# Optimization experiments

Measured on AMD Instinct MI355X. Metric: run time of the kernel, lower is better.

The kernel has to match this reference:

```python
import jax, jax.numpy as jnp
import numpy as np

B, C, CI, H, W = 4, 256, 128, 64, 64  # batch, in_channels, inter_channels, spatial
EPS = 1e-5


def conv1x1(x, w, b):
    # x: [b,c,h,w], w: [o,c], b: [o] -> [b,o,h,w]
    return jnp.einsum('bchw,oc->bohw', x, w) + b[None, :, None, None]


def setup_inputs() -> dict:
    key = jax.random.key(0)
    ks = jax.random.split(key, 16)
    s_in = 1.0 / np.sqrt(C)
    s_mid = 1.0 / np.sqrt(CI)
    inp = {
        'feats_all': jax.random.normal(ks[0], (B, C, H, W), dtype=jnp.float32),
        'human_feats': jax.random.normal(ks[1], (B, C, H, W), dtype=jnp.float32),
        'g_w': jax.random.uniform(ks[2], (CI, C), jnp.float32, -s_in, s_in),
        'g_b': jax.random.uniform(ks[3], (CI,), jnp.float32, -s_in, s_in),
        'theta_w': jax.random.uniform(ks[4], (CI, C), jnp.float32, -s_in, s_in),
        'theta_b': jax.random.uniform(ks[5], (CI,), jnp.float32, -s_in, s_in),
        'phi_w': jax.random.uniform(ks[6], (CI, C), jnp.float32, -s_in, s_in),
        'phi_b': jax.random.uniform(ks[7], (CI,), jnp.float32, -s_in, s_in),
        'human_theta_w': jax.random.uniform(ks[8], (CI, C), jnp.float32, -s_in, s_in),
        'human_theta_b': jax.random.uniform(ks[9], (CI,), jnp.float32, -s_in, s_in),
        'human_phi_w': jax.random.uniform(ks[10], (CI, C), jnp.float32, -s_in, s_in),
        'human_phi_b': jax.random.uniform(ks[11], (CI,), jnp.float32, -s_in, s_in),
        'W_w': jax.random.uniform(ks[12], (C, CI), jnp.float32, -s_mid, s_mid),
        'W_b': jax.random.uniform(ks[13], (C,), jnp.float32, -s_mid, s_mid),
        'bn_gamma': jax.random.normal(ks[14], (C,), dtype=jnp.float32) * 0.1 + 1.0,
        'bn_beta': jax.random.normal(ks[15], (C,), dtype=jnp.float32) * 0.1,
        'bn_mean': jnp.zeros((C,), jnp.float32),
        'bn_var': jnp.ones((C,), jnp.float32),
    }
    return inp


def reference(feats_all, human_feats, g_w, g_b, theta_w, theta_b, phi_w, phi_b,
              human_theta_w, human_theta_b, human_phi_w, human_phi_b,
              W_w, W_b, bn_gamma, bn_beta, bn_mean, bn_var):
    b = feats_all.shape[0]
    n = H * W
    scale = CI ** -0.5

    # human attention map: softmax over keys of scaled QK^T
    hq = conv1x1(human_feats, human_theta_w, human_theta_b).reshape(b, CI, n)  # [b,ci,n]
    hk = conv1x1(human_feats, human_phi_w, human_phi_b).reshape(b, CI, n)
    human_map = jax.nn.softmax(scale * jnp.einsum('bcq,bck->bqk', hq, hk), axis=-1)

    # standard non-local map on feats_all
    th = conv1x1(feats_all, theta_w, theta_b).reshape(b, CI, n)
    ph = conv1x1(feats_all, phi_w, phi_b).reshape(b, CI, n)
    f = jax.nn.softmax(scale * jnp.einsum('bcq,bck->bqk', th, ph), axis=-1)

    g_x = conv1x1(feats_all, g_w, g_b).reshape(b, CI, n)  # [b,ci,n]

    attn = (human_map + f) * 0.5                          # [b,n,n]
    y = jnp.einsum('bqk,bck->bcq', attn, g_x)             # [b,ci,n]
    y = y.reshape(b, CI, H, W)

    wy = conv1x1(y, W_w, W_b)                             # [b,C,H,W]
    # BatchNorm2d (eval mode, running stats)
    inv = bn_gamma / jnp.sqrt(bn_var + EPS)
    out = (wy - bn_mean[None, :, None, None]) * inv[None, :, None, None] + bn_beta[None, :, None, None]
    return out
```

## Files before the change

kernel.cpp:

```cpp
#include <hip/hip_runtime.h>

#define DEVI __device__ __forceinline__

typedef float f32x4 __attribute__((ext_vector_type(4)));
typedef float f32x16 __attribute__((ext_vector_type(16)));
typedef unsigned int u32x4 __attribute__((ext_vector_type(4)));
typedef unsigned int u32x2 __attribute__((ext_vector_type(2)));
typedef __bf16 bf16x8 __attribute__((ext_vector_type(8)));

#define NB 4
#define CIN 256
#define CI_ 128
#define NN 4096
#define QSCALE 0.12752792233895158f

typedef unsigned short us;

DEVI us f2bf(float f) {
  unsigned int x = __float_as_uint(f);
  x += 0x7FFFu + ((x >> 16) & 1u);
  return (us)(x >> 16);
}

DEVI unsigned cvtpk(float lo, float hi) {
  unsigned r;
  asm("v_cvt_pk_bf16_f32 %0, %1, %2" : "=v"(r) : "v"(lo), "v"(hi));
  return r;
}

DEVI void plswap(unsigned& a, unsigned& b) {
  asm volatile("v_permlane32_swap_b32 %0, %1" : "+v"(a), "+v"(b));
}

DEVI float exp2fast(float x) {
#if __has_builtin(__builtin_amdgcn_exp2f)
  return __builtin_amdgcn_exp2f(x);
#else
  return exp2f(x);
#endif
}

DEVI f32x4 mfma16(u32x4 a, u32x4 b, f32x4 c) {
  return __builtin_amdgcn_mfma_f32_16x16x32_bf16(
      __builtin_bit_cast(bf16x8, a), __builtin_bit_cast(bf16x8, b), c, 0, 0, 0);
}

DEVI f32x16 mfma32(u32x4 a, u32x4 b, f32x16 c) {
  return __builtin_amdgcn_mfma_f32_32x32x16_bf16(
      __builtin_bit_cast(bf16x8, a), __builtin_bit_cast(bf16x8, b), c, 0, 0, 0);
}

DEVI void gload16(const void* g, void* l) {
  __builtin_amdgcn_global_load_lds(
      (const __attribute__((address_space(1))) void*)g,
      (__attribute__((address_space(3))) void*)l, 16, 0, 0);
}

DEVI void softpack(f32x16& a, float& ls, u32x4* pa) {
#pragma unroll
  for (int r = 0; r < 16; ++r) {
    float e = exp2fast(a[r]);
    ls += e;
    a[r] = e;
  }
  unsigned x0 = cvtpk(a[0], a[1]), z0 = cvtpk(a[2], a[3]);
  unsigned y0 = cvtpk(a[4], a[5]), t0 = cvtpk(a[6], a[7]);
  plswap(x0, y0);
  plswap(z0, t0);
  pa[0][0] = x0; pa[0][1] = z0; pa[0][2] = y0; pa[0][3] = t0;
  unsigned x1 = cvtpk(a[8], a[9]), z1 = cvtpk(a[10], a[11]);
  unsigned y1 = cvtpk(a[12], a[13]), t1 = cvtpk(a[14], a[15]);
  plswap(x1, y1);
  plswap(z1, t1);
  pa[1][0] = x1; pa[1][1] = z1; pa[1][2] = y1; pa[1][3] = t1;
}

__global__ __launch_bounds__(256) void wcvt_kernel(
    const float* __restrict__ hth_w, const float* __restrict__ hph_w,
    const float* __restrict__ th_w, const float* __restrict__ ph_w,
    const float* __restrict__ g_w, const float* __restrict__ Ww,
    us* __restrict__ wb) {
  const float* srcs[6] = {hth_w, hph_w, th_w, ph_w, g_w, Ww};
  const float* s = srcs[blockIdx.y];
  us* d = wb + blockIdx.y * 32768;
  int idx = (blockIdx.x * 256 + threadIdx.x) * 4;
  f32x4 v = *(const f32x4*)(s + idx);
  u32x2 o;
  o[0] = cvtpk(v[0], v[1]);
  o[1] = cvtpk(v[2], v[3]);
  *(u32x2*)(d + idx) = o;
}

__global__ __launch_bounds__(256) void proj_kernel(
    const float* __restrict__ feats, const float* __restrict__ human,
    const float* __restrict__ g_b, const float* __restrict__ th_b,
    const float* __restrict__ ph_b, const float* __restrict__ hth_b,
    const float* __restrict__ hph_b, const us* __restrict__ wb,
    us* __restrict__ hqT, us* __restrict__ hkT,
    us* __restrict__ thT, us* __restrict__ phT, us* __restrict__ gP) {
  __shared__ alignas(16) us xf[64 * 256];
  __shared__ alignas(16) us xh[64 * 256];
  const int t = threadIdx.x;
  const int b = blockIdx.y;
  const int n0 = blockIdx.x * 64;
  const int w = t >> 6, l = t & 63, g16 = l >> 4, l15 = l & 15;
  const int tg = t >> 4, tl = t & 15;

  for (int which = 0; which < 2; ++which) {
    const float* src = which ? human : feats;
    us* dst = which ? xh : xf;
#pragma unroll
    for (int i = 0; i < 8; ++i) {
      int p = i * 16 + tg;
      const float* s0 = src + (size_t)(b * CIN + 2 * p) * NN + n0 + tl * 4;
      f32x4 v0 = *(const f32x4*)s0;
      f32x4 v1 = *(const f32x4*)(s0 + NN);
#pragma unroll
      for (int j = 0; j < 4; ++j) {
        int row = tl * 4 + j;
        *(unsigned*)((char*)dst + row * 512 + ((4 * p) ^ ((row & 15) << 4))) =
            cvtpk(v0[j], v1[j]);
      }
    }
  }
  __syncthreads();

  const float* pb[4] = {hth_b, hph_b, th_b, ph_b};
  us* pout[4] = {hqT, hkT, thT, phT};

  u32x4 afrag[8];
  const int arow = w * 16 + l15;
  for (int p = 0; p < 4; ++p) {
    const us* tile = (p < 2) ? xh : xf;
    if (p == 0 || p == 2) {
#pragma unroll
      for (int s = 0; s < 8; ++s)
        afrag[s] = *(const u32x4*)((const char*)tile + arow * 512 +
                                   (((s << 6) | (g16 << 4)) ^ (l15 << 4)));
    }
    const us* wbp = wb + p * 32768;
    const float scl = (p == 0 || p == 2) ? QSCALE : 1.0f;
    for (int nt = 0; nt < 8; ++nt) {
      f32x4 acc = {0.f, 0.f, 0.f, 0.f};
#pragma unroll
      for (int s = 0; s < 8; ++s) {
        u32x4 bf = *(const u32x4*)(wbp + (nt * 16 + l15) * 256 + s * 32 + g16 * 8);
        acc = mfma16(afrag[s], bf, acc);
      }
      float bias = pb[p][nt * 16 + l15];
#pragma unroll
      for (int r = 0; r < 4; ++r) {
        int nrow = n0 + w * 16 + g16 * 4 + r;
        pout[p][((size_t)b * NN + nrow) * CI_ + nt * 16 + l15] =
            f2bf((acc[r] + bias) * scl);
      }
    }
  }

  const us* wbg = wb + 4 * 32768;
  u32x4 ag[2][8];
#pragma unroll
  for (int mt = 0; mt < 2; ++mt)
#pragma unroll
    for (int s = 0; s < 8; ++s)
      ag[mt][s] = *(const u32x4*)(wbg + (w * 32 + mt * 16 + l15) * 256 + s * 32 + g16 * 8);
  float gb[2][4];
#pragma unroll
  for (int mt = 0; mt < 2; ++mt)
#pragma unroll
    for (int r = 0; r < 4; ++r) gb[mt][r] = g_b[w * 32 + mt * 16 + g16 * 4 + r];
  for (int nt = 0; nt < 4; ++nt) {
    f32x4 acc0 = {0.f, 0.f, 0.f, 0.f}, acc1 = {0.f, 0.f, 0.f, 0.f};
#pragma unroll
    for (int s = 0; s < 8; ++s) {
      u32x4 bf = *(const u32x4*)((const char*)xf + (nt * 16 + l15) * 512 +
                                 ((s * 64 + g16 * 16) ^ (l15 << 4)));
      acc0 = mfma16(ag[0][s], bf, acc0);
      acc1 = mfma16(ag[1][s], bf, acc1);
    }
#pragma unroll
    for (int r = 0; r < 4; ++r) {
      int ci0 = w * 32 + g16 * 4 + r;
      gP[((size_t)b * CI_ + ci0) * NN + n0 + nt * 16 + l15] = f2bf(acc0[r] + gb[0][r]);
      gP[((size_t)b * CI_ + ci0 + 16) * NN + n0 + nt * 16 + l15] = f2bf(acc1[r] + gb[1][r]);
    }
  }
}

__global__ __launch_bounds__(128, 2) void attn_kernel(
    const us* __restrict__ hqT, const us* __restrict__ hkT,
    const us* __restrict__ thT, const us* __restrict__ phT,
    const us* __restrict__ gP, us* __restrict__ PY, float* __restrict__ PL) {
  __shared__ alignas(16) us sK[2][32 * 128];
  __shared__ alignas(16) us sV[2][32 * 128];

  const int t = threadIdx.x, w = t >> 6, l = t & 63;
  const int l31 = l & 31, hi = l >> 5, l15 = l & 15;
  const int id = blockIdx.x;
  const int bp = id & 7, b = bp & 3, path = bp >> 2;
  const int r2 = id >> 3, h = r2 & 1, chunk = r2 >> 1;
  const int qw = chunk * 64 + w * 32, kb = h * 2048;
  const us* Qs = (path ? thT : hqT) + (size_t)b * NN * CI_;
  const char* Kb = (const char*)((path ? phT : hkT) + (size_t)b * NN * CI_);
  const char* Vb = (const char*)(gP + (size_t)b * CI_ * NN);

  u32x4 aQ[8];
#pragma unroll
  for (int s = 0; s < 8; ++s)
    aQ[s] = *(const u32x4*)(Qs + (size_t)(qw + l31) * CI_ + s * 16 + hi * 8);

  f32x16 Y[4];
#pragma unroll
  for (int ds = 0; ds < 4; ++ds) Y[ds] = 0.f;
  float lsum = 0.f;

  const int sr = l >> 4;

  auto stage = [&](int k0, int buf) {
#pragma unroll
    for (int i = 0; i < 4; ++i) {
      int row = w * 16 + i * 4 + sr;
      gload16(Kb + (size_t)(k0 + row) * 256 + (((l & 15) ^ (row & 15)) << 4),
              (char*)sK[buf] + (w * 16 + i * 4) * 256);
    }
#pragma unroll
    for (int i = 0; i < 4; ++i) {
      int R = w * 16 + i * 4 + sr;
      int lu = (l & 15) ^ (R & 15);
      int d = 4 * R + (lu >> 2);
      gload16(Vb + (size_t)d * 8192 + (size_t)k0 * 2 + (lu & 3) * 16,
              (char*)sV[buf] + (w * 16 + i * 4) * 256);
    }
  };

  stage(kb, 0);
  __syncthreads();

  for (int kt = 0; kt < 64; ++kt) {
    const int cur = kt & 1;
    if (kt < 63) stage(kb + (kt + 1) * 32, cur ^ 1);
    const char* kt_ = (const char*)sK[cur];
    const char* vt_ = (const char*)sV[cur];

    f32x16 a0 = 0.f;
    __builtin_amdgcn_s_setprio(1);
#pragma unroll
    for (int s = 0; s < 8; ++s) {
      u32x4 ak = *(const u32x4*)(kt_ + l31 * 256 + (((s * 2 + hi) ^ l15) << 4));
      a0 = mfma32(ak, aQ[s], a0);
    }
    __builtin_amdgcn_s_setprio(0);

    u32x4 pa[2];
    softpack(a0, lsum, pa);

    __builtin_amdgcn_s_setprio(1);
#pragma unroll
    for (int ds = 0; ds < 4; ++ds) {
      int R = ds * 8 + (l31 >> 2);
      const char* vb = vt_ + R * 256;
      int k_ = R & 15;
      u32x4 v0 = *(const u32x4*)(vb + ((((l31 & 3) * 4 + hi) ^ k_) << 4));
      u32x4 v1 = *(const u32x4*)(vb + ((((l31 & 3) * 4 + 2 + hi) ^ k_) << 4));
      Y[ds] = mfma32(pa[0], v0, Y[ds]);
      Y[ds] = mfma32(pa[1], v1, Y[ds]);
    }
    __builtin_amdgcn_s_setprio(0);
    __syncthreads();
  }

  lsum += __shfl_xor(lsum, 32);
  if (hi == 0) PL[(size_t)(h * 8 + bp) * NN + qw + l31] = lsum;

  float* buf = (float*)(w ? (us*)sV : (us*)sK);
#pragma unroll
  for (int ds = 0; ds < 4; ++ds) {
    int d = ds * 32 + l31;
#pragma unroll
    for (int m = 0; m < 4; ++m) {
      f32x4 v = {Y[ds][4 * m], Y[ds][4 * m + 1], Y[ds][4 * m + 2],
                 Y[ds][4 * m + 3]};
      *(f32x4*)((char*)buf + d * 128 + (((2 * m + hi) ^ (d & 7)) << 4)) = v;
    }
  }
  float yv[64];
#pragma unroll
  for (int j = 0; j < 64; ++j) {
    int d = hi * 64 + j;
    yv[j] = *(const float*)((char*)buf + d * 128 +
                            ((((l31 >> 2) ^ (d & 7)) << 4)) + (l31 & 3) * 4);
  }
  us* dst = PY + ((size_t)(h * 8 + bp) * NN + qw + l31) * CI_ + hi * 64;
#pragma unroll
  for (int o = 0; o < 8; ++o) {
    u32x4 pk;
#pragma unroll
    for (int e = 0; e < 4; ++e)
      pk[e] = cvtpk(yv[o * 8 + 2 * e], yv[o * 8 + 2 * e + 1]);
    *(u32x4*)(dst + o * 8) = pk;
  }
}

__global__ __launch_bounds__(256) void wout_kernel(
    const us* __restrict__ PY, const float* __restrict__ PL,
    const us* __restrict__ wb, const float* __restrict__ Wb,
    const float* __restrict__ gamma, const float* __restrict__ beta,
    const float* __restrict__ mean, const float* __restrict__ var,
    float* __restrict__ out) {
  __shared__ alignas(16) us sY[64 * 128];
  const int t = threadIdx.x, w = t >> 6, l = t & 63, g16 = l >> 4, l15 = l & 15;
  const int n0 = blockIdx.x * 64;
  const int ob = blockIdx.y * 64;
  const int b = blockIdx.z;

  {
    const int row = t >> 2, cg = t & 3;
    const int n = n0 + row;
    float acc[32];
#pragma unroll
    for (int e = 0; e < 32; ++e) acc[e] = 0.f;
#pragma unroll
    for (int p = 0; p < 2; ++p) {
      int bpi = p * 4 + b;
      float sc = 0.5f / (PL[(size_t)bpi * NN + n] + PL[(size_t)(8 + bpi) * NN + n]);
#pragma unroll
      for (int hh = 0; hh < 2; ++hh) {
        const us* src = PY + (size_t)(hh * 8 + bpi) * (NN * CI_) +
                        (size_t)n * CI_ + cg * 32;
#pragma unroll
        for (int j = 0; j < 4; ++j) {
          u32x4 v = *(const u32x4*)(src + j * 8);
#pragma unroll
          for (int e = 0; e < 4; ++e) {
            unsigned u = v[e];
            acc[j * 8 + 2 * e] += __uint_as_float(u << 16) * sc;
            acc[j * 8 + 2 * e + 1] += __uint_as_float(u & 0xFFFF0000u) * sc;
          }
        }
      }
    }
#pragma unroll
    for (int j = 0; j < 4; ++j) {
      u32x4 o;
#pragma unroll
      for (int e = 0; e < 4; ++e)
        o[e] = cvtpk(acc[j * 8 + 2 * e], acc[j * 8 + 2 * e + 1]);
      *(u32x4*)((char*)sY + row * 256 + ((cg * 64 + j * 16) ^ ((row & 7) << 4))) = o;
    }
  }

  const us* wbw = wb + 5 * 32768;
  u32x4 aW[4];
  const int orow = ob + w * 16 + l15;
#pragma unroll
  for (int s = 0; s < 4; ++s)
    aW[s] = *(const u32x4*)(wbw + orow * 128 + s * 32 + g16 * 8);
  float wbias[4], inv_[4], mu[4], bt[4];
#pragma unroll
  for (int r = 0; r < 4; ++r) {
    int o = ob + w * 16 + g16 * 4 + r;
    wbias[r] = Wb[o];
    inv_[r] = gamma[o] * rsqrtf(var[o] + 1e-5f);
    mu[r] = mean[o];
    bt[r] = beta[o];
  }
  __syncthreads();

  for (int nt = 0; nt < 4; ++nt) {
    f32x4 acc = {0.f, 0.f, 0.f, 0.f};
#pragma unroll
    for (int s = 0; s < 4; ++s) {
      u32x4 bf = *(const u32x4*)((const char*)sY + (nt * 16 + l15) * 256 +
                                 (((s << 6) | (g16 << 4)) ^ ((l15 & 7) << 4)));
      acc = mfma16(aW[s], bf, acc);
    }
#pragma unroll
    for (int r = 0; r < 4; ++r) {
      int o = ob + w * 16 + g16 * 4 + r;
      out[((size_t)b * CIN + o) * NN + n0 + nt * 16 + l15] =
          (acc[r] + wbias[r] - mu[r]) * inv_[r] + bt[r];
    }
  }
}

extern "C" void kernel_launch(void* const* d_in, const int* in_sizes, int n_in,
                              void* d_out, int out_size, void* d_ws, size_t ws_size,
                              hipStream_t stream) {
  const float* feats = (const float*)d_in[0];
  const float* human = (const float*)d_in[1];
  const float* g_w = (const float*)d_in[2];
  const float* g_b = (const float*)d_in[3];
  const float* th_w = (const float*)d_in[4];
  const float* th_b = (const float*)d_in[5];
  const float* ph_w = (const float*)d_in[6];
  const float* ph_b = (const float*)d_in[7];
  const float* hth_w = (const float*)d_in[8];
  const float* hth_b = (const float*)d_in[9];
  const float* hph_w = (const float*)d_in[10];
  const float* hph_b = (const float*)d_in[11];
  const float* Ww = (const float*)d_in[12];
  const float* Wb = (const float*)d_in[13];
  const float* gamma = (const float*)d_in[14];
  const float* beta = (const float*)d_in[15];
  const float* mean = (const float*)d_in[16];
  const float* var = (const float*)d_in[17];

  us* ws = (us*)d_ws;
  const size_t SZ = (size_t)NB * NN * CI_;
  us* hqT = ws;
  us* hkT = ws + SZ;
  us* thT = ws + 2 * SZ;
  us* phT = ws + 3 * SZ;
  us* gP = ws + 4 * SZ;
  us* PY = ws + 5 * SZ;
  float* PL = (float*)(ws + 5 * SZ + 8388608);
  us* wb = ws + 5 * SZ + 8388608 + 131072;

  wcvt_kernel<<<dim3(32, 6), 256, 0, stream>>>(hth_w, hph_w, th_w, ph_w, g_w, Ww, wb);
  proj_kernel<<<dim3(64, 4), 256, 0, stream>>>(feats, human, g_b, th_b, ph_b,
                                               hth_b, hph_b, wb, hqT, hkT, thT,
                                               phT, gP);
  attn_kernel<<<1024, 128, 0, stream>>>(hqT, hkT, thT, phT, gP, PY, PL);
  wout_kernel<<<dim3(64, 4, 4), 256, 0, stream>>>(PY, PL, wb, Wb, gamma, beta,
                                                  mean, var, (float*)d_out);
}
```

Baseline: 144.1 us.

## Load V tiles straight into registers instead of staging through LDS

The attention kernel now loads the V (g) operand for the next key tile directly from global memory into registers, double-buffered across two register arrays with a manually unrolled pair of iterations, rather than staging it through shared memory. This removes the LDS writes and reads for V. In exchange it raises register pressure, and each wave now fetches its own copy of V from global memory. It also precomputes the K shared-memory offsets and reorganises the softmax row-sum into a tree reduction to shorten the dependency chain.

```diff
diff --git a/kernel.cpp b/kernel.cpp
--- a/kernel.cpp
+++ b/kernel.cpp
@@ -58,11 +58,12 @@
 
 DEVI void softpack(f32x16& a, float& ls, u32x4* pa) {
 #pragma unroll
-  for (int r = 0; r < 16; ++r) {
-    float e = exp2fast(a[r]);
-    ls += e;
-    a[r] = e;
-  }
+  for (int r = 0; r < 16; ++r) a[r] = exp2fast(a[r]);
+  float s0 = (a[0] + a[1]) + (a[2] + a[3]);
+  float s1 = (a[4] + a[5]) + (a[6] + a[7]);
+  float s2 = (a[8] + a[9]) + (a[10] + a[11]);
+  float s3 = (a[12] + a[13]) + (a[14] + a[15]);
+  ls += (s0 + s1) + (s2 + s3);
   unsigned x0 = cvtpk(a[0], a[1]), z0 = cvtpk(a[2], a[3]);
   unsigned y0 = cvtpk(a[4], a[5]), t0 = cvtpk(a[6], a[7]);
   plswap(x0, y0);
@@ -192,7 +193,7 @@
     const us* __restrict__ thT, const us* __restrict__ phT,
     const us* __restrict__ gP, us* __restrict__ PY, float* __restrict__ PL) {
   __shared__ alignas(16) us sK[2][32 * 128];
-  __shared__ alignas(16) us sV[2][32 * 128];
+  __shared__ alignas(16) us sX[2][32 * 128];
 
   const int t = threadIdx.x, w = t >> 6, l = t & 63;
   const int l31 = l & 31, hi = l >> 5, l15 = l & 15;
@@ -209,6 +210,10 @@
   for (int s = 0; s < 8; ++s)
     aQ[s] = *(const u32x4*)(Qs + (size_t)(qw + l31) * CI_ + s * 16 + hi * 8);
 
+  int koff[8];
+#pragma unroll
+  for (int s = 0; s < 8; ++s) koff[s] = l31 * 256 + (((s * 2 + hi) ^ l15) << 4);
+
   f32x16 Y[4];
 #pragma unroll
   for (int ds = 0; ds < 4; ++ds) Y[ds] = 0.f;
@@ -216,63 +221,63 @@
 
   const int sr = l >> 4;
 
-  auto stage = [&](int k0, int buf) {
+  auto stageK = [&](int k0, int buf) {
 #pragma unroll
     for (int i = 0; i < 4; ++i) {
       int row = w * 16 + i * 4 + sr;
       gload16(Kb + (size_t)(k0 + row) * 256 + (((l & 15) ^ (row & 15)) << 4),
               (char*)sK[buf] + (w * 16 + i * 4) * 256);
     }
-#pragma unroll
-    for (int i = 0; i < 4; ++i) {
-      int R = w * 16 + i * 4 + sr;
-      int lu = (l & 15) ^ (R & 15);
-      int d = 4 * R + (lu >> 2);
-      gload16(Vb + (size_t)d * 8192 + (size_t)k0 * 2 + (lu & 3) * 16,
-              (char*)sV[buf] + (w * 16 + i * 4) * 256);
-    }
   };
-
-  stage(kb, 0);
+  auto vloadV = [&](int k0, u32x4 (&vn)[8]) {
+#pragma unroll
+    for (int ds = 0; ds < 4; ++ds) {
+      const char* p = Vb + (size_t)(ds * 32 + l31) * 8192 + (size_t)k0 * 2 + hi * 16;
+      vn[2 * ds] = *(const u32x4*)p;
+      vn[2 * ds + 1] = *(const u32x4*)(p + 32);
+    }
+  };
+
+  u32x4 vA[8], vB[8];
+  stageK(kb, 0);
+  vloadV(kb, vA);
   __syncthreads();
 
-  for (int kt = 0; kt < 64; ++kt) {
-    const int cur = kt & 1;
-    if (kt < 63) stage(kb + (kt + 1) * 32, cur ^ 1);
+  auto iter = [&](int kt, int cur, u32x4 (&vc)[8], u32x4 (&vn)[8]) {
+    if (kt < 63) {
+      stageK(kb + (kt + 1) * 32, cur ^ 1);
+      vloadV(kb + (kt + 1) * 32, vn);
+    }
     const char* kt_ = (const char*)sK[cur];
-    const char* vt_ = (const char*)sV[cur];
-
     f32x16 a0 = 0.f;
     __builtin_amdgcn_s_setprio(1);
 #pragma unroll
     for (int s = 0; s < 8; ++s) {
-      u32x4 ak = *(const u32x4*)(kt_ + l31 * 256 + (((s * 2 + hi) ^ l15) << 4));
+      u32x4 ak = *(const u32x4*)(kt_ + koff[s]);
       a0 = mfma32(ak, aQ[s], a0);
     }
     __builtin_amdgcn_s_setprio(0);
-
     u32x4 pa[2];
     softpack(a0, lsum, pa);
-
     __builtin_amdgcn_s_setprio(1);
 #pragma unroll
     for (int ds = 0; ds < 4; ++ds) {
-      int R = ds * 8 + (l31 >> 2);
-      const char* vb = vt_ + R * 256;
-      int k_ = R & 15;
-      u32x4 v0 = *(const u32x4*)(vb + ((((l31 & 3) * 4 + hi) ^ k_) << 4));
-      u32x4 v1 = *(const u32x4*)(vb + ((((l31 & 3) * 4 + 2 + hi) ^ k_) << 4));
-      Y[ds] = mfma32(pa[0], v0, Y[ds]);
-      Y[ds] = mfma32(pa[1], v1, Y[ds]);
+      Y[ds] = mfma32(pa[0], vc[2 * ds], Y[ds]);
+      Y[ds] = mfma32(pa[1], vc[2 * ds + 1], Y[ds]);
     }
     __builtin_amdgcn_s_setprio(0);
     __syncthreads();
+  };
+
+  for (int kt2 = 0; kt2 < 32; ++kt2) {
+    iter(2 * kt2, 0, vA, vB);
+    iter(2 * kt2 + 1, 1, vB, vA);
   }
 
   lsum += __shfl_xor(lsum, 32);
   if (hi == 0) PL[(size_t)(h * 8 + bp) * NN + qw + l31] = lsum;
 
-  float* buf = (float*)(w ? (us*)sV : (us*)sK);
+  float* buf = (float*)(w ? (us*)sX : (us*)sK);
 #pragma unroll
   for (int ds = 0; ds < 4; ++ds) {
     int d = ds * 32 + l31;
```

Result: slower. 203.0 us (+40.9%).

## Split projection kernel by input across blocks; fuse output-channel tiles in wout

Applied to the files above, without the earlier changes.

The projection kernel now launches twice as many blocks, one per input tensor (human or feats), with each block staging a single 32KB bf16 tile in LDS instead of two. This raises parallelism and cuts per-block LDS. The wout kernel now loops over all four 64-channel output tiles inside one block. The PY reduction and softmax normalization are therefore done once per position instead of being repeated for each output tile, though there are fewer blocks in flight. The feats block does more work than the human block because it also computes g, so load is imbalanced.

```diff
diff --git a/kernel.cpp b/kernel.cpp
--- a/kernel.cpp
+++ b/kernel.cpp
@@ -98,48 +98,43 @@
     const float* __restrict__ hph_b, const us* __restrict__ wb,
     us* __restrict__ hqT, us* __restrict__ hkT,
     us* __restrict__ thT, us* __restrict__ phT, us* __restrict__ gP) {
-  __shared__ alignas(16) us xf[64 * 256];
-  __shared__ alignas(16) us xh[64 * 256];
+  __shared__ alignas(16) us xt[64 * 256];
   const int t = threadIdx.x;
   const int b = blockIdx.y;
   const int n0 = blockIdx.x * 64;
+  const int grp = blockIdx.z;
   const int w = t >> 6, l = t & 63, g16 = l >> 4, l15 = l & 15;
   const int tg = t >> 4, tl = t & 15;
 
-  for (int which = 0; which < 2; ++which) {
-    const float* src = which ? human : feats;
-    us* dst = which ? xh : xf;
-#pragma unroll
-    for (int i = 0; i < 8; ++i) {
-      int p = i * 16 + tg;
-      const float* s0 = src + (size_t)(b * CIN + 2 * p) * NN + n0 + tl * 4;
-      f32x4 v0 = *(const f32x4*)s0;
-      f32x4 v1 = *(const f32x4*)(s0 + NN);
-#pragma unroll
-      for (int j = 0; j < 4; ++j) {
-        int row = tl * 4 + j;
-        *(unsigned*)((char*)dst + row * 512 + ((4 * p) ^ ((row & 15) << 4))) =
-            cvtpk(v0[j], v1[j]);
-      }
+  const float* src = grp ? feats : human;
+#pragma unroll
+  for (int i = 0; i < 8; ++i) {
+    int p = i * 16 + tg;
+    const float* s0 = src + (size_t)(b * CIN + 2 * p) * NN + n0 + tl * 4;
+    f32x4 v0 = *(const f32x4*)s0;
+    f32x4 v1 = *(const f32x4*)(s0 + NN);
+#pragma unroll
+    for (int j = 0; j < 4; ++j) {
+      int row = tl * 4 + j;
+      *(unsigned*)((char*)xt + row * 512 + ((4 * p) ^ ((row & 15) << 4))) =
+          cvtpk(v0[j], v1[j]);
     }
   }
   __syncthreads();
 
-  const float* pb[4] = {hth_b, hph_b, th_b, ph_b};
-  us* pout[4] = {hqT, hkT, thT, phT};
+  const float* pb2[2] = {grp ? th_b : hth_b, grp ? ph_b : hph_b};
+  us* pout2[2] = {grp ? thT : hqT, grp ? phT : hkT};
+  const us* wb0 = wb + grp * 2 * 32768;
 
   u32x4 afrag[8];
   const int arow = w * 16 + l15;
-  for (int p = 0; p < 4; ++p) {
-    const us* tile = (p < 2) ? xh : xf;
-    if (p == 0 || p == 2) {
-#pragma unroll
-      for (int s = 0; s < 8; ++s)
-        afrag[s] = *(const u32x4*)((const char*)tile + arow * 512 +
-                                   (((s << 6) | (g16 << 4)) ^ (l15 << 4)));
-    }
-    const us* wbp = wb + p * 32768;
-    const float scl = (p == 0 || p == 2) ? QSCALE : 1.0f;
+#pragma unroll
+  for (int s = 0; s < 8; ++s)
+    afrag[s] = *(const u32x4*)((const char*)xt + arow * 512 +
+                               (((s << 6) | (g16 << 4)) ^ (l15 << 4)));
+  for (int p = 0; p < 2; ++p) {
+    const us* wbp = wb0 + p * 32768;
+    const float scl = (p == 0) ? QSCALE : 1.0f;
     for (int nt = 0; nt < 8; ++nt) {
       f32x4 acc = {0.f, 0.f, 0.f, 0.f};
 #pragma unroll
@@ -147,42 +142,44 @@
         u32x4 bf = *(const u32x4*)(wbp + (nt * 16 + l15) * 256 + s * 32 + g16 * 8);
         acc = mfma16(afrag[s], bf, acc);
       }
-      float bias = pb[p][nt * 16 + l15];
+      float bias = pb2[p][nt * 16 + l15];
 #pragma unroll
       for (int r = 0; r < 4; ++r) {
         int nrow = n0 + w * 16 + g16 * 4 + r;
-        pout[p][((size_t)b * NN + nrow) * CI_ + nt * 16 + l15] =
+        pout2[p][((size_t)b * NN + nrow) * CI_ + nt * 16 + l15] =
             f2bf((acc[r] + bias) * scl);
       }
     }
   }
 
-  const us* wbg = wb + 4 * 32768;
-  u32x4 ag[2][8];
-#pragma unroll
-  for (int mt = 0; mt < 2; ++mt)
-#pragma unroll
-    for (int s = 0; s < 8; ++s)
-      ag[mt][s] = *(const u32x4*)(wbg + (w * 32 + mt * 16 + l15) * 256 + s * 32 + g16 * 8);
-  float gb[2][4];
-#pragma unroll
-  for (int mt = 0; mt < 2; ++mt)
-#pragma unroll
-    for (int r = 0; r < 4; ++r) gb[mt][r] = g_b[w * 32 + mt * 16 + g16 * 4 + r];
-  for (int nt = 0; nt < 4; ++nt) {
-    f32x4 acc0 = {0.f, 0.f, 0.f, 0.f}, acc1 = {0.f, 0.f, 0.f, 0.f};
-#pragma unroll
-    for (int s = 0; s < 8; ++s) {
-      u32x4 bf = *(const u32x4*)((const char*)xf + (nt * 16 + l15) * 512 +
-                                 ((s * 64 + g16 * 16) ^ (l15 << 4)));
-      acc0 = mfma16(ag[0][s], bf, acc0);
-      acc1 = mfma16(ag[1][s], bf, acc1);
-    }
-#pragma unroll
-    for (int r = 0; r < 4; ++r) {
-      int ci0 = w * 32 + g16 * 4 + r;
-      gP[((size_t)b * CI_ + ci0) * NN + n0 + nt * 16 + l15] = f2bf(acc0[r] + gb[0][r]);
-      gP[((size_t)b * CI_ + ci0 + 16) * NN + n0 + nt * 16 + l15] = f2bf(acc1[r] + gb[1][r]);
+  if (grp) {
+    const us* wbg = wb + 4 * 32768;
+    u32x4 ag[2][8];
+#pragma unroll
+    for (int mt = 0; mt < 2; ++mt)
+#pragma unroll
+      for (int s = 0; s < 8; ++s)
+        ag[mt][s] = *(const u32x4*)(wbg + (w * 32 + mt * 16 + l15) * 256 + s * 32 + g16 * 8);
+    float gb[2][4];
+#pragma unroll
+    for (int mt = 0; mt < 2; ++mt)
+#pragma unroll
+      for (int r = 0; r < 4; ++r) gb[mt][r] = g_b[w * 32 + mt * 16 + g16 * 4 + r];
+    for (int nt = 0; nt < 4; ++nt) {
+      f32x4 acc0 = {0.f, 0.f, 0.f, 0.f}, acc1 = {0.f, 0.f, 0.f, 0.f};
+#pragma unroll
+      for (int s = 0; s < 8; ++s) {
+        u32x4 bf = *(const u32x4*)((const char*)xt + (nt * 16 + l15) * 512 +
+                                   ((s * 64 + g16 * 16) ^ (l15 << 4)));
+        acc0 = mfma16(ag[0][s], bf, acc0);
+        acc1 = mfma16(ag[1][s], bf, acc1);
+      }
+#pragma unroll
+      for (int r = 0; r < 4; ++r) {
+        int ci0 = w * 32 + g16 * 4 + r;
+        gP[((size_t)b * CI_ + ci0) * NN + n0 + nt * 16 + l15] = f2bf(acc0[r] + gb[0][r]);
+        gP[((size_t)b * CI_ + ci0 + 16) * NN + n0 + nt * 16 + l15] = f2bf(acc1[r] + gb[1][r]);
+      }
     }
   }
 }
@@ -310,8 +307,7 @@
   __shared__ alignas(16) us sY[64 * 128];
   const int t = threadIdx.x, w = t >> 6, l = t & 63, g16 = l >> 4, l15 = l & 15;
   const int n0 = blockIdx.x * 64;
-  const int ob = blockIdx.y * 64;
-  const int b = blockIdx.z;
+  const int b = blockIdx.y;
 
   {
     const int row = t >> 2, cg = t & 3;
@@ -348,37 +344,40 @@
       *(u32x4*)((char*)sY + row * 256 + ((cg * 64 + j * 16) ^ ((row & 7) << 4))) = o;
     }
   }
+  __syncthreads();
 
   const us* wbw = wb + 5 * 32768;
-  u32x4 aW[4];
-  const int orow = ob + w * 16 + l15;
-#pragma unroll
-  for (int s = 0; s < 4; ++s)
-    aW[s] = *(const u32x4*)(wbw + orow * 128 + s * 32 + g16 * 8);
-  float wbias[4], inv_[4], mu[4], bt[4];
-#pragma unroll
-  for (int r = 0; r < 4; ++r) {
-    int o = ob + w * 16 + g16 * 4 + r;
-    wbias[r] = Wb[o];
-    inv_[r] = gamma[o] * rsqrtf(var[o] + 1e-5f);
-    mu[r] = mean[o];
-    bt[r] = beta[o];
-  }
-  __syncthreads();
-
-  for (int nt = 0; nt < 4; ++nt) {
-    f32x4 acc = {0.f, 0.f, 0.f, 0.f};
-#pragma unroll
-    for (int s = 0; s < 4; ++s) {
-      u32x4 bf = *(const u32x4*)((const char*)sY + (nt * 16 + l15) * 256 +
-                                 (((s << 6) | (g16 << 4)) ^ ((l15 & 7) << 4)));
-      acc = mfma16(aW[s], bf, acc);
-    }
+  for (int ob4 = 0; ob4 < 4; ++ob4) {
+    const int ob = ob4 * 64;
+    u32x4 aW[4];
+    const int orow = ob + w * 16 + l15;
+#pragma unroll
+    for (int s = 0; s < 4; ++s)
+      aW[s] = *(const u32x4*)(wbw + orow * 128 + s * 32 + g16 * 8);
+    float wbias[4], inv_[4], mu[4], bt[4];
 #pragma unroll
     for (int r = 0; r < 4; ++r) {
       int o = ob + w * 16 + g16 * 4 + r;
-      out[((size_t)b * CIN + o) * NN + n0 + nt * 16 + l15] =
-          (acc[r] + wbias[r] - mu[r]) * inv_[r] + bt[r];
+      wbias[r] = Wb[o];
+      inv_[r] = gamma[o] * rsqrtf(var[o] + 1e-5f);
+      mu[r] = mean[o];
+      bt[r] = beta[o];
+    }
+
+    for (int nt = 0; nt < 4; ++nt) {
+      f32x4 acc = {0.f, 0.f, 0.f, 0.f};
+#pragma unroll
+      for (int s = 0; s < 4; ++s) {
+        u32x4 bf = *(const u32x4*)((const char*)sY + (nt * 16 + l15) * 256 +
+                                   (((s << 6) | (g16 << 4)) ^ ((l15 & 7) << 4)));
+        acc = mfma16(aW[s], bf, acc);
+      }
+#pragma unroll
+      for (int r = 0; r < 4; ++r) {
+        int o = ob + w * 16 + g16 * 4 + r;
+        out[((size_t)b * CIN + o) * NN + n0 + nt * 16 + l15] =
+            (acc[r] + wbias[r] - mu[r]) * inv_[r] + bt[r];
+      }
     }
   }
 }
@@ -417,10 +416,10 @@
   us* wb = ws + 5 * SZ + 8388608 + 131072;
 
   wcvt_kernel<<<dim3(32, 6), 256, 0, stream>>>(hth_w, hph_w, th_w, ph_w, g_w, Ww, wb);
-  proj_kernel<<<dim3(64, 4), 256, 0, stream>>>(feats, human, g_b, th_b, ph_b,
-                                               hth_b, hph_b, wb, hqT, hkT, thT,
-                                               phT, gP);
+  proj_kernel<<<dim3(64, 4, 2), 256, 0, stream>>>(feats, human, g_b, th_b, ph_b,
+                                                  hth_b, hph_b, wb, hqT, hkT,
+                                                  thT, phT, gP);
   attn_kernel<<<1024, 128, 0, stream>>>(hqT, hkT, thT, phT, gP, PY, PL);
-  wout_kernel<<<dim3(64, 4, 4), 256, 0, stream>>>(PY, PL, wb, Wb, gamma, beta,
-                                                  mean, var, (float*)d_out);
-}
+  wout_kernel<<<dim3(64, 4), 256, 0, stream>>>(PY, PL, wb, Wb, gamma, beta,
+                                               mean, var, (float*)d_out);
+}
```

Result: faster. 136.3 us (-5.4%).
